# Kernel optimization log

Measured on AMD Instinct MI355X. Metric: run time of the kernel, lower is better.

Reference implementation:

```python
import jax, jax.numpy as jnp
import numpy as np

NEG_BIG = -9.0e15

def setup_inputs() -> dict:
    key = jax.random.key(0)
    k1, k2, k3, k4 = jax.random.split(key, 4)
    N, F_in, F_out = 2048, 512, 64
    x = jax.random.normal(k1, (N, F_in), dtype=jnp.float32)
    adj = jax.random.randint(k2, (N, N), 0, 2, dtype=jnp.int32)
    # xavier_uniform with gain=1.414
    def xavier(k, shape, gain=1.414):
        fan_in, fan_out = shape[0], shape[1]
        bound = gain * np.sqrt(6.0 / (fan_in + fan_out))
        return jax.random.uniform(k, shape, jnp.float32, -bound, bound)
    W = xavier(k3, (F_in, F_out))
    a = xavier(k4, (F_out, 1))
    return {"x": x, "adj": adj, "W": W, "a": a}

def reference(x, adj, W, a):
    h = x @ W                                  # [N, F_out]
    # pairwise |h_i - h_j| projected by a: e[i,j] = relu(sum_f |h_i,f - h_j,f| * a_f)
    diff = jnp.abs(h[:, None, :] - h[None, :, :])   # [N, N, F_out]
    e = jax.nn.relu(jnp.einsum('ijf,fo->ij', diff, a))  # [N, N]
    scores = jnp.where(adj > 0, e, NEG_BIG)
    attention = jax.nn.softmax(scores, axis=1)
    out = attention @ h                        # [N, F_out]
    return jax.nn.relu(out)                    # concat=True path
```

## Files before the change

kernel.cpp:

```cpp
#include <hip/hip_runtime.h>

#define Nn 2048
#define FIN 512
#define FO 64
#define SHIFT 20.0f
#define NJT 32
#define HS 68
#define PTS 68
#define ZTOT (Nn * FO + Nn)

#define HX(r, f) ((r) * HS + ((((f) >> 2) ^ (((r) >> 2) & 15)) << 2))

__global__ __launch_bounds__(256) void gat_xw(const float* __restrict__ x,
                                              const float* __restrict__ W,
                                              float* __restrict__ h,
                                              float* __restrict__ z) {
    const int gt = blockIdx.x * 256 + threadIdx.x;
    if (z != nullptr && gt < ZTOT) z[gt] = 0.f;

    __shared__ float part[2][2][FO];
    const int wave = threadIdx.x >> 6;
    const int lane = threadIdx.x & 63;
    const int rs = wave >> 1;
    const int kh = wave & 1;
    int row = blockIdx.x * 2 + rs;
    row = __builtin_amdgcn_readfirstlane(row);
    const float* xr = x + (size_t)row * FIN + kh * (FIN / 2);
    const float* Wp = W + (size_t)kh * (FIN / 2) * FO;
    float acc = 0.f;
#pragma unroll 2
    for (int k = 0; k < FIN / 2; k += 8) {
        float4 xa = *(const float4*)(xr + k);
        float4 xb = *(const float4*)(xr + k + 4);
        acc = fmaf(xa.x, Wp[(k + 0) * FO + lane], acc);
        acc = fmaf(xa.y, Wp[(k + 1) * FO + lane], acc);
        acc = fmaf(xa.z, Wp[(k + 2) * FO + lane], acc);
        acc = fmaf(xa.w, Wp[(k + 3) * FO + lane], acc);
        acc = fmaf(xb.x, Wp[(k + 4) * FO + lane], acc);
        acc = fmaf(xb.y, Wp[(k + 5) * FO + lane], acc);
        acc = fmaf(xb.z, Wp[(k + 6) * FO + lane], acc);
        acc = fmaf(xb.w, Wp[(k + 7) * FO + lane], acc);
    }
    part[rs][kh][lane] = acc;
    __syncthreads();
    if (threadIdx.x < 128) {
        const int r2 = threadIdx.x >> 6;
        const int l2 = threadIdx.x & 63;
        h[((size_t)blockIdx.x * 2 + r2) * FO + l2] = part[r2][0][l2] + part[r2][1][l2];
    }
}

template <bool ATOMIC>
__global__ __launch_bounds__(256, 4) void gat_attn6(const float* __restrict__ h,
                                                    const int* __restrict__ adj,
                                                    const float* __restrict__ a,
                                                    float* __restrict__ po,
                                                    float* __restrict__ pl) {
    __shared__ __align__(16) float hj_s[64 * HS];
    __shared__ __align__(16) float pT_s[64 * PTS];

    const int tid = threadIdx.x;
    const int w = tid >> 6;
    const int lane = tid & 63;
    const int li = lane & 3;
    const int lj = lane >> 2;
    const int it = blockIdx.x >> 5;
    const int jt = blockIdx.x & (NJT - 1);
    const int ib = it * 64;
    const int jb = jt * 64;
    const int iw = w * 16;

    for (int g4 = tid; g4 < 1024; g4 += 256) {
        const int row = g4 >> 4;
        const int f0 = (g4 & 15) * 4;
        float4 u = *(const float4*)(h + (size_t)jb * FO + (size_t)g4 * 4);
        *(float4*)&hj_s[HX(row, f0)] = u;
    }
    __syncthreads();

    float e[4][4];
#pragma unroll
    for (int di = 0; di < 4; di++)
#pragma unroll
        for (int dj = 0; dj < 4; dj++) e[di][dj] = 0.f;

    const float* hib = h + (size_t)(ib + iw + 4 * li) * FO;

#pragma unroll 4
    for (int f4 = 0; f4 < 16; f4++) {
        const float4 av = *(const float4*)(a + f4 * 4);
        float4 hi4[4], hj4[4];
#pragma unroll
        for (int d = 0; d < 4; d++) {
            hi4[d] = *(const float4*)(hib + (size_t)d * FO + f4 * 4);
            hj4[d] = *(const float4*)&hj_s[HX(4 * lj + d, f4 * 4)];
        }
#pragma unroll
        for (int di = 0; di < 4; di++)
#pragma unroll
            for (int dj = 0; dj < 4; dj++) {
                e[di][dj] = fmaf(fabsf(hi4[di].x - hj4[dj].x), av.x, e[di][dj]);
                e[di][dj] = fmaf(fabsf(hi4[di].y - hj4[dj].y), av.y, e[di][dj]);
                e[di][dj] = fmaf(fabsf(hi4[di].z - hj4[dj].z), av.z, e[di][dj]);
                e[di][dj] = fmaf(fabsf(hi4[di].w - hj4[dj].w), av.w, e[di][dj]);
            }
    }

    float ls[4];
#pragma unroll
    for (int di = 0; di < 4; di++) ls[di] = 0.f;
#pragma unroll
    for (int di = 0; di < 4; di++) {
        const int4 am = *(const int4*)(adj + (size_t)(ib + iw + 4 * li + di) * Nn + (jb + 4 * lj));
        const int* ap = (const int*)&am;
#pragma unroll
        for (int dj = 0; dj < 4; dj++) {
            const float p = (ap[dj] > 0) ? __expf(fmaxf(e[di][dj], 0.f) - SHIFT) : 0.f;
            e[di][dj] = p;
            ls[di] += p;
        }
    }

#pragma unroll
    for (int dj = 0; dj < 4; dj++) {
        *(float4*)&pT_s[(4 * lj + dj) * PTS + iw + 4 * li] =
            make_float4(e[0][dj], e[1][dj], e[2][dj], e[3][dj]);
    }

    float pv[4][4];
#pragma unroll
    for (int u = 0; u < 4; u++)
#pragma unroll
        for (int v2 = 0; v2 < 4; v2++) pv[u][v2] = 0.f;

#pragma unroll 4
    for (int j = 0; j < 64; j++) {
        const float4 pj = *(const float4*)&pT_s[j * PTS + iw + 4 * li];
        const float4 hv = *(const float4*)(h + (size_t)(jb + j) * FO + 4 * lj);
        pv[0][0] = fmaf(pj.x, hv.x, pv[0][0]);
        pv[0][1] = fmaf(pj.x, hv.y, pv[0][1]);
        pv[0][2] = fmaf(pj.x, hv.z, pv[0][2]);
        pv[0][3] = fmaf(pj.x, hv.w, pv[0][3]);
        pv[1][0] = fmaf(pj.y, hv.x, pv[1][0]);
        pv[1][1] = fmaf(pj.y, hv.y, pv[1][1]);
        pv[1][2] = fmaf(pj.y, hv.z, pv[1][2]);
        pv[1][3] = fmaf(pj.y, hv.w, pv[1][3]);
        pv[2][0] = fmaf(pj.z, hv.x, pv[2][0]);
        pv[2][1] = fmaf(pj.z, hv.y, pv[2][1]);
        pv[2][2] = fmaf(pj.z, hv.z, pv[2][2]);
        pv[2][3] = fmaf(pj.z, hv.w, pv[2][3]);
        pv[3][0] = fmaf(pj.w, hv.x, pv[3][0]);
        pv[3][1] = fmaf(pj.w, hv.y, pv[3][1]);
        pv[3][2] = fmaf(pj.w, hv.z, pv[3][2]);
        pv[3][3] = fmaf(pj.w, hv.w, pv[3][3]);
    }

#pragma unroll
    for (int di = 0; di < 4; di++) {
        float v = ls[di];
        v += __shfl_xor(v, 4, 64);
        v += __shfl_xor(v, 8, 64);
        v += __shfl_xor(v, 16, 64);
        v += __shfl_xor(v, 32, 64);
        ls[di] = v;
    }

    if constexpr (!ATOMIC) {
        if (lj == 0) {
#pragma unroll
            for (int di = 0; di < 4; di++)
                pl[(size_t)jt * Nn + (ib + iw + 4 * li + di)] = ls[di];
        }
#pragma unroll
        for (int di = 0; di < 4; di++)
            *(float4*)&po[((size_t)jt * Nn + (ib + iw + 4 * li + di)) * FO + 4 * lj] =
                make_float4(pv[di][0], pv[di][1], pv[di][2], pv[di][3]);
    } else {
        if (lj == 0) {
#pragma unroll
            for (int di = 0; di < 4; di++)
                atomicAdd(&pl[ib + iw + 4 * li + di], ls[di]);
        }
#pragma unroll
        for (int di = 0; di < 4; di++) {
#pragma unroll
            for (int v2 = 0; v2 < 4; v2++)
                atomicAdd(&po[(size_t)(ib + iw + 4 * li + di) * FO + 4 * lj + v2], pv[di][v2]);
        }
    }
}

__global__ __launch_bounds__(256) void gat_reduce(const float* __restrict__ po,
                                                  const float* __restrict__ pl,
                                                  float* __restrict__ out) {
    const int t = blockIdx.x * 256 + threadIdx.x;
    const int i = t >> 6;
    float s = 0.f;
#pragma unroll
    for (int p = 0; p < NJT; p++) s += po[(size_t)p * (Nn * FO) + t];
    float l = 0.f;
#pragma unroll
    for (int p = 0; p < NJT; p++) l += pl[p * Nn + i];
    out[t] = fmaxf(s / l, 0.f);
}

__global__ __launch_bounds__(256) void gat_fin(const float* __restrict__ osum,
                                               const float* __restrict__ lsum,
                                               float* __restrict__ out) {
    const int t = blockIdx.x * 256 + threadIdx.x;
    out[t] = fmaxf(osum[t] / lsum[t >> 6], 0.f);
}

extern "C" void kernel_launch(void* const* d_in, const int* in_sizes, int n_in,
                              void* d_out, int out_size, void* d_ws, size_t ws_size,
                              hipStream_t stream) {
    const float* x   = (const float*)d_in[0];
    const int*   adj = (const int*)d_in[1];
    const float* W   = (const float*)d_in[2];
    const float* a   = (const float*)d_in[3];
    float* out = (float*)d_out;

    float* h = (float*)d_ws;
    const size_t need = ((size_t)Nn * FO + (size_t)NJT * Nn * FO + (size_t)NJT * Nn) * 4;

    if (ws_size >= need) {
        float* po = h + (size_t)Nn * FO;
        float* pl = po + (size_t)NJT * Nn * FO;
        gat_xw<<<dim3(1024), dim3(256), 0, stream>>>(x, W, h, nullptr);
        gat_attn6<false><<<dim3(32 * NJT), dim3(256), 0, stream>>>(h, adj, a, po, pl);
        gat_reduce<<<dim3(512), dim3(256), 0, stream>>>(po, pl, out);
    } else {
        float* osum = h + (size_t)Nn * FO;
        float* lsum = osum + (size_t)Nn * FO;
        gat_xw<<<dim3(1024), dim3(256), 0, stream>>>(x, W, h, osum);
        gat_attn6<true><<<dim3(32 * NJT), dim3(256), 0, stream>>>(h, adj, a, osum, lsum);
        gat_fin<<<dim3(512), dim3(256), 0, stream>>>(osum, lsum, out);
    }
}
```

Measured before the change: 133.7 us.

## Enlarge attention i-tile to 128 rows and stage hi, a, and hj in LDS

The attention kernel now covers 128 query rows per block instead of 64, and each thread computes an 8x4 score tile instead of 4x4. The h_i rows, the vector a, and the h_j rows used in the P·V product are now staged in shared memory, so the per-thread global loads go away and each loaded h_j tile is reused across twice as many rows. The P^T buffer reuses the h_i region behind an extra barrier and gets a new XOR swizzle. In exchange the block count halves (512 blocks), register pressure roughly doubles under the launch bounds of 4 waves, and shared-memory use per block grows, which may cut occupancy.

```diff
diff --git a/kernel.cpp b/kernel.cpp
--- a/kernel.cpp
+++ b/kernel.cpp
@@ -6,10 +6,12 @@
 #define SHIFT 20.0f
 #define NJT 32
 #define HS 68
-#define PTS 68
+#define PTS2 132
 #define ZTOT (Nn * FO + Nn)
 
-#define HX(r, f) ((r) * HS + ((((f) >> 2) ^ (((r) >> 2) & 15)) << 2))
+#define HXI(r, f) ((r) * HS + ((((f) >> 2) ^ (((r) >> 3) & 15)) << 2))
+#define HXJ(r, f) ((r) * HS + ((((f) >> 2) ^ (((r) >> 2) & 15)) << 2))
+#define PX(j, i)  ((j) * PTS2 + ((((i) >> 2) ^ ((j) & 7)) << 2))
 
 __global__ __launch_bounds__(256) void gat_xw(const float* __restrict__ x,
                                               const float* __restrict__ W,
@@ -51,13 +53,16 @@
 }
 
 template <bool ATOMIC>
-__global__ __launch_bounds__(256, 4) void gat_attn6(const float* __restrict__ h,
+__global__ __launch_bounds__(256, 4) void gat_attn7(const float* __restrict__ h,
                                                     const int* __restrict__ adj,
                                                     const float* __restrict__ a,
                                                     float* __restrict__ po,
                                                     float* __restrict__ pl) {
+    __shared__ __align__(16) float up[128 * HS];
     __shared__ __align__(16) float hj_s[64 * HS];
-    __shared__ __align__(16) float pT_s[64 * PTS];
+    __shared__ float a_s[FO];
+    float* hi_s = up;
+    float* pT_s = up;
 
     const int tid = threadIdx.x;
     const int w = tid >> 6;
@@ -66,37 +71,39 @@
     const int lj = lane >> 2;
     const int it = blockIdx.x >> 5;
     const int jt = blockIdx.x & (NJT - 1);
-    const int ib = it * 64;
+    const int ib = it * 128;
     const int jb = jt * 64;
-    const int iw = w * 16;
-
+    const int i0 = 32 * w + 8 * li;
+
+    for (int g4 = tid; g4 < 2048; g4 += 256) {
+        const int row = g4 >> 4;
+        const int f0 = (g4 & 15) * 4;
+        *(float4*)&hi_s[HXI(row, f0)] = *(const float4*)(h + (size_t)ib * FO + (size_t)g4 * 4);
+    }
     for (int g4 = tid; g4 < 1024; g4 += 256) {
         const int row = g4 >> 4;
         const int f0 = (g4 & 15) * 4;
-        float4 u = *(const float4*)(h + (size_t)jb * FO + (size_t)g4 * 4);
-        *(float4*)&hj_s[HX(row, f0)] = u;
-    }
+        *(float4*)&hj_s[HXJ(row, f0)] = *(const float4*)(h + (size_t)jb * FO + (size_t)g4 * 4);
+    }
+    if (tid < FO) a_s[tid] = a[tid];
     __syncthreads();
 
-    float e[4][4];
-#pragma unroll
-    for (int di = 0; di < 4; di++)
+    float e[8][4];
+#pragma unroll
+    for (int di = 0; di < 8; di++)
 #pragma unroll
         for (int dj = 0; dj < 4; dj++) e[di][dj] = 0.f;
-
-    const float* hib = h + (size_t)(ib + iw + 4 * li) * FO;
 
 #pragma unroll 4
     for (int f4 = 0; f4 < 16; f4++) {
-        const float4 av = *(const float4*)(a + f4 * 4);
-        float4 hi4[4], hj4[4];
-#pragma unroll
-        for (int d = 0; d < 4; d++) {
-            hi4[d] = *(const float4*)(hib + (size_t)d * FO + f4 * 4);
-            hj4[d] = *(const float4*)&hj_s[HX(4 * lj + d, f4 * 4)];
-        }
-#pragma unroll
-        for (int di = 0; di < 4; di++)
+        const float4 av = *(const float4*)&a_s[f4 * 4];
+        float4 hi4[8], hj4[4];
+#pragma unroll
+        for (int d = 0; d < 8; d++) hi4[d] = *(const float4*)&hi_s[HXI(i0 + d, f4 * 4)];
+#pragma unroll
+        for (int d = 0; d < 4; d++) hj4[d] = *(const float4*)&hj_s[HXJ(4 * lj + d, f4 * 4)];
+#pragma unroll
+        for (int di = 0; di < 8; di++)
 #pragma unroll
             for (int dj = 0; dj < 4; dj++) {
                 e[di][dj] = fmaf(fabsf(hi4[di].x - hj4[dj].x), av.x, e[di][dj]);
@@ -106,12 +113,12 @@
             }
     }
 
-    float ls[4];
-#pragma unroll
-    for (int di = 0; di < 4; di++) ls[di] = 0.f;
-#pragma unroll
-    for (int di = 0; di < 4; di++) {
-        const int4 am = *(const int4*)(adj + (size_t)(ib + iw + 4 * li + di) * Nn + (jb + 4 * lj));
+    float ls[8];
+#pragma unroll
+    for (int di = 0; di < 8; di++) ls[di] = 0.f;
+#pragma unroll
+    for (int di = 0; di < 8; di++) {
+        const int4 am = *(const int4*)(adj + (size_t)(ib + i0 + di) * Nn + (jb + 4 * lj));
         const int* ap = (const int*)&am;
 #pragma unroll
         for (int dj = 0; dj < 4; dj++) {
@@ -121,42 +128,48 @@
         }
     }
 
+    __syncthreads();
+
 #pragma unroll
     for (int dj = 0; dj < 4; dj++) {
-        *(float4*)&pT_s[(4 * lj + dj) * PTS + iw + 4 * li] =
+        const int j = 4 * lj + dj;
+        *(float4*)&pT_s[PX(j, i0)] =
             make_float4(e[0][dj], e[1][dj], e[2][dj], e[3][dj]);
-    }
-
-    float pv[4][4];
-#pragma unroll
-    for (int u = 0; u < 4; u++)
-#pragma unroll
-        for (int v2 = 0; v2 < 4; v2++) pv[u][v2] = 0.f;
+        *(float4*)&pT_s[PX(j, i0 + 4)] =
+            make_float4(e[4][dj], e[5][dj], e[6][dj], e[7][dj]);
+    }
+
+    float pv[8][4];
+#pragma unroll
+    for (int di = 0; di < 8; di++)
+#pragma unroll
+        for (int c = 0; c < 4; c++) pv[di][c] = 0.f;
 
 #pragma unroll 4
     for (int j = 0; j < 64; j++) {
-        const float4 pj = *(const float4*)&pT_s[j * PTS + iw + 4 * li];
-        const float4 hv = *(const float4*)(h + (size_t)(jb + j) * FO + 4 * lj);
-        pv[0][0] = fmaf(pj.x, hv.x, pv[0][0]);
-        pv[0][1] = fmaf(pj.x, hv.y, pv[0][1]);
-        pv[0][2] = fmaf(pj.x, hv.z, pv[0][2]);
-        pv[0][3] = fmaf(pj.x, hv.w, pv[0][3]);
-        pv[1][0] = fmaf(pj.y, hv.x, pv[1][0]);
-        pv[1][1] = fmaf(pj.y, hv.y, pv[1][1]);
-        pv[1][2] = fmaf(pj.y, hv.z, pv[1][2]);
-        pv[1][3] = fmaf(pj.y, hv.w, pv[1][3]);
-        pv[2][0] = fmaf(pj.z, hv.x, pv[2][0]);
-        pv[2][1] = fmaf(pj.z, hv.y, pv[2][1]);
-        pv[2][2] = fmaf(pj.z, hv.z, pv[2][2]);
-        pv[2][3] = fmaf(pj.z, hv.w, pv[2][3]);
-        pv[3][0] = fmaf(pj.w, hv.x, pv[3][0]);
-        pv[3][1] = fmaf(pj.w, hv.y, pv[3][1]);
-        pv[3][2] = fmaf(pj.w, hv.z, pv[3][2]);
-        pv[3][3] = fmaf(pj.w, hv.w, pv[3][3]);
-    }
-
-#pragma unroll
-    for (int di = 0; di < 4; di++) {
+        const float4 pj0 = *(const float4*)&pT_s[PX(j, i0)];
+        const float4 pj1 = *(const float4*)&pT_s[PX(j, i0 + 4)];
+        const float4 hv = *(const float4*)&hj_s[HXJ(j, 4 * lj)];
+        pv[0][0] = fmaf(pj0.x, hv.x, pv[0][0]); pv[0][1] = fmaf(pj0.x, hv.y, pv[0][1]);
+        pv[0][2] = fmaf(pj0.x, hv.z, pv[0][2]); pv[0][3] = fmaf(pj0.x, hv.w, pv[0][3]);
+        pv[1][0] = fmaf(pj0.y, hv.x, pv[1][0]); pv[1][1] = fmaf(pj0.y, hv.y, pv[1][1]);
+        pv[1][2] = fmaf(pj0.y, hv.z, pv[1][2]); pv[1][3] = fmaf(pj0.y, hv.w, pv[1][3]);
+        pv[2][0] = fmaf(pj0.z, hv.x, pv[2][0]); pv[2][1] = fmaf(pj0.z, hv.y, pv[2][1]);
+        pv[2][2] = fmaf(pj0.z, hv.z, pv[2][2]); pv[2][3] = fmaf(pj0.z, hv.w, pv[2][3]);
+        pv[3][0] = fmaf(pj0.w, hv.x, pv[3][0]); pv[3][1] = fmaf(pj0.w, hv.y, pv[3][1]);
+        pv[3][2] = fmaf(pj0.w, hv.z, pv[3][2]); pv[3][3] = fmaf(pj0.w, hv.w, pv[3][3]);
+        pv[4][0] = fmaf(pj1.x, hv.x, pv[4][0]); pv[4][1] = fmaf(pj1.x, hv.y, pv[4][1]);
+        pv[4][2] = fmaf(pj1.x, hv.z, pv[4][2]); pv[4][3] = fmaf(pj1.x, hv.w, pv[4][3]);
+        pv[5][0] = fmaf(pj1.y, hv.x, pv[5][0]); pv[5][1] = fmaf(pj1.y, hv.y, pv[5][1]);
+        pv[5][2] = fmaf(pj1.y, hv.z, pv[5][2]); pv[5][3] = fmaf(pj1.y, hv.w, pv[5][3]);
+        pv[6][0] = fmaf(pj1.z, hv.x, pv[6][0]); pv[6][1] = fmaf(pj1.z, hv.y, pv[6][1]);
+        pv[6][2] = fmaf(pj1.z, hv.z, pv[6][2]); pv[6][3] = fmaf(pj1.z, hv.w, pv[6][3]);
+        pv[7][0] = fmaf(pj1.w, hv.x, pv[7][0]); pv[7][1] = fmaf(pj1.w, hv.y, pv[7][1]);
+        pv[7][2] = fmaf(pj1.w, hv.z, pv[7][2]); pv[7][3] = fmaf(pj1.w, hv.w, pv[7][3]);
+    }
+
+#pragma unroll
+    for (int di = 0; di < 8; di++) {
         float v = ls[di];
         v += __shfl_xor(v, 4, 64);
         v += __shfl_xor(v, 8, 64);
@@ -168,24 +181,24 @@
     if constexpr (!ATOMIC) {
         if (lj == 0) {
 #pragma unroll
-            for (int di = 0; di < 4; di++)
-                pl[(size_t)jt * Nn + (ib + iw + 4 * li + di)] = ls[di];
-        }
-#pragma unroll
-        for (int di = 0; di < 4; di++)
-            *(float4*)&po[((size_t)jt * Nn + (ib + iw + 4 * li + di)) * FO + 4 * lj] =
+            for (int di = 0; di < 8; di++)
+                pl[(size_t)jt * Nn + (ib + i0 + di)] = ls[di];
+        }
+#pragma unroll
+        for (int di = 0; di < 8; di++)
+            *(float4*)&po[((size_t)jt * Nn + (ib + i0 + di)) * FO + 4 * lj] =
                 make_float4(pv[di][0], pv[di][1], pv[di][2], pv[di][3]);
     } else {
         if (lj == 0) {
 #pragma unroll
-            for (int di = 0; di < 4; di++)
-                atomicAdd(&pl[ib + iw + 4 * li + di], ls[di]);
-        }
-#pragma unroll
-        for (int di = 0; di < 4; di++) {
-#pragma unroll
-            for (int v2 = 0; v2 < 4; v2++)
-                atomicAdd(&po[(size_t)(ib + iw + 4 * li + di) * FO + 4 * lj + v2], pv[di][v2]);
+            for (int di = 0; di < 8; di++)
+                atomicAdd(&pl[ib + i0 + di], ls[di]);
+        }
+#pragma unroll
+        for (int di = 0; di < 8; di++) {
+#pragma unroll
+            for (int c = 0; c < 4; c++)
+                atomicAdd(&po[(size_t)(ib + i0 + di) * FO + 4 * lj + c], pv[di][c]);
         }
     }
 }
@@ -227,13 +240,13 @@
         float* po = h + (size_t)Nn * FO;
         float* pl = po + (size_t)NJT * Nn * FO;
         gat_xw<<<dim3(1024), dim3(256), 0, stream>>>(x, W, h, nullptr);
-        gat_attn6<false><<<dim3(32 * NJT), dim3(256), 0, stream>>>(h, adj, a, po, pl);
+        gat_attn7<false><<<dim3(16 * NJT), dim3(256), 0, stream>>>(h, adj, a, po, pl);
         gat_reduce<<<dim3(512), dim3(256), 0, stream>>>(po, pl, out);
     } else {
         float* osum = h + (size_t)Nn * FO;
         float* lsum = osum + (size_t)Nn * FO;
         gat_xw<<<dim3(1024), dim3(256), 0, stream>>>(x, W, h, osum);
-        gat_attn6<true><<<dim3(32 * NJT), dim3(256), 0, stream>>>(h, adj, a, osum, lsum);
+        gat_attn7<true><<<dim3(16 * NJT), dim3(256), 0, stream>>>(h, adj, a, osum, lsum);
         gat_fin<<<dim3(512), dim3(256), 0, stream>>>(osum, lsum, out);
     }
 }
```

Measured after the change: 121.5 us. -9.1%, faster.

## Exploit symmetry of pairwise L1 scores to compute each tile pair once

Applied to the files above, without the earlier changes.

The score e[i,j] depends on |h_i - h_j|, so it is symmetric. The kernel now launches only upper-triangular tile pairs and reuses each computed e tile for both (i,j) and (j,i), masking with adj and adj-transposed. The block index is mapped to (it,jt) with a triangular-number inversion. Both h tiles are now staged in shared memory so the PV products read h from LDS, which raises LDS use per block to four 64x68 buffers and may reduce occupancy. Off-diagonal blocks now do twice the PV work and an extra adj transpose read, with a second pass after a barrier.

```diff
diff --git a/kernel.cpp b/kernel.cpp
--- a/kernel.cpp
+++ b/kernel.cpp
@@ -4,7 +4,8 @@
 #define FIN 512
 #define FO 64
 #define SHIFT 20.0f
-#define NJT 32
+#define NP 32
+#define NB ((NP * (NP + 1)) / 2)
 #define HS 68
 #define PTS 68
 #define ZTOT (Nn * FO + Nn)
@@ -51,21 +52,29 @@
 }
 
 template <bool ATOMIC>
-__global__ __launch_bounds__(256, 4) void gat_attn6(const float* __restrict__ h,
+__global__ __launch_bounds__(256, 4) void gat_attn9(const float* __restrict__ h,
                                                     const int* __restrict__ adj,
                                                     const float* __restrict__ a,
                                                     float* __restrict__ po,
                                                     float* __restrict__ pl) {
+    __shared__ __align__(16) float hi_s[64 * HS];
     __shared__ __align__(16) float hj_s[64 * HS];
-    __shared__ __align__(16) float pT_s[64 * PTS];
+    __shared__ __align__(16) float pTa[64 * PTS];
+    __shared__ __align__(16) float pTb[64 * PTS];
+    __shared__ float a_s[FO];
+
+    const int b = blockIdx.x;
+    int it = (int)((65.0f - sqrtf(4225.0f - 8.0f * (float)b)) * 0.5f);
+    while ((it + 1) * NP - (((it + 1) * it) >> 1) <= b) it++;
+    while (it * NP - ((it * (it - 1)) >> 1) > b) it--;
+    const int jt = it + (b - (it * NP - ((it * (it - 1)) >> 1)));
+    const bool diag = (it == jt);
 
     const int tid = threadIdx.x;
     const int w = tid >> 6;
     const int lane = tid & 63;
     const int li = lane & 3;
     const int lj = lane >> 2;
-    const int it = blockIdx.x >> 5;
-    const int jt = blockIdx.x & (NJT - 1);
     const int ib = it * 64;
     const int jb = jt * 64;
     const int iw = w * 16;
@@ -73,9 +82,10 @@
     for (int g4 = tid; g4 < 1024; g4 += 256) {
         const int row = g4 >> 4;
         const int f0 = (g4 & 15) * 4;
-        float4 u = *(const float4*)(h + (size_t)jb * FO + (size_t)g4 * 4);
-        *(float4*)&hj_s[HX(row, f0)] = u;
-    }
+        *(float4*)&hi_s[HX(row, f0)] = *(const float4*)(h + (size_t)ib * FO + (size_t)g4 * 4);
+        *(float4*)&hj_s[HX(row, f0)] = *(const float4*)(h + (size_t)jb * FO + (size_t)g4 * 4);
+    }
+    if (tid < FO) a_s[tid] = a[tid];
     __syncthreads();
 
     float e[4][4];
@@ -83,16 +93,14 @@
     for (int di = 0; di < 4; di++)
 #pragma unroll
         for (int dj = 0; dj < 4; dj++) e[di][dj] = 0.f;
-
-    const float* hib = h + (size_t)(ib + iw + 4 * li) * FO;
 
 #pragma unroll 4
     for (int f4 = 0; f4 < 16; f4++) {
-        const float4 av = *(const float4*)(a + f4 * 4);
+        const float4 av = *(const float4*)&a_s[f4 * 4];
         float4 hi4[4], hj4[4];
 #pragma unroll
         for (int d = 0; d < 4; d++) {
-            hi4[d] = *(const float4*)(hib + (size_t)d * FO + f4 * 4);
+            hi4[d] = *(const float4*)&hi_s[HX(iw + 4 * li + d, f4 * 4)];
             hj4[d] = *(const float4*)&hj_s[HX(4 * lj + d, f4 * 4)];
         }
 #pragma unroll
@@ -106,25 +114,42 @@
             }
     }
 
-    float ls[4];
-#pragma unroll
-    for (int di = 0; di < 4; di++) ls[di] = 0.f;
+#pragma unroll
+    for (int di = 0; di < 4; di++)
+#pragma unroll
+        for (int dj = 0; dj < 4; dj++)
+            e[di][dj] = __expf(fmaxf(e[di][dj], 0.f) - SHIFT);
+
+    int4 ama[4];
+#pragma unroll
+    for (int di = 0; di < 4; di++)
+        ama[di] = *(const int4*)(adj + (size_t)(ib + iw + 4 * li + di) * Nn + (jb + 4 * lj));
+#define PA(di, dj) ((((const int*)&ama[di])[dj] > 0) ? e[di][dj] : 0.f)
+
+    float lsa[4];
 #pragma unroll
     for (int di = 0; di < 4; di++) {
-        const int4 am = *(const int4*)(adj + (size_t)(ib + iw + 4 * li + di) * Nn + (jb + 4 * lj));
-        const int* ap = (const int*)&am;
-#pragma unroll
-        for (int dj = 0; dj < 4; dj++) {
-            const float p = (ap[dj] > 0) ? __expf(fmaxf(e[di][dj], 0.f) - SHIFT) : 0.f;
-            e[di][dj] = p;
-            ls[di] += p;
-        }
-    }
-
+        lsa[di] = 0.f;
+#pragma unroll
+        for (int dj = 0; dj < 4; dj++) lsa[di] += PA(di, dj);
+    }
 #pragma unroll
     for (int dj = 0; dj < 4; dj++) {
-        *(float4*)&pT_s[(4 * lj + dj) * PTS + iw + 4 * li] =
-            make_float4(e[0][dj], e[1][dj], e[2][dj], e[3][dj]);
+        *(float4*)&pTa[(4 * lj + dj) * PTS + iw + 4 * li] =
+            make_float4(PA(0, dj), PA(1, dj), PA(2, dj), PA(3, dj));
+    }
+
+    if (!diag) {
+        int4 amb[4];
+#pragma unroll
+        for (int dj = 0; dj < 4; dj++)
+            amb[dj] = *(const int4*)(adj + (size_t)(jb + 4 * lj + dj) * Nn + (ib + iw + 4 * li));
+#define PB(di, dj) ((((const int*)&amb[dj])[di] > 0) ? e[di][dj] : 0.f)
+#pragma unroll
+        for (int di = 0; di < 4; di++) {
+            *(float4*)&pTb[(iw + 4 * li + di) * PTS + 4 * lj] =
+                make_float4(PB(di, 0), PB(di, 1), PB(di, 2), PB(di, 3));
+        }
     }
 
     float pv[4][4];
@@ -135,41 +160,32 @@
 
 #pragma unroll 4
     for (int j = 0; j < 64; j++) {
-        const float4 pj = *(const float4*)&pT_s[j * PTS + iw + 4 * li];
-        const float4 hv = *(const float4*)(h + (size_t)(jb + j) * FO + 4 * lj);
-        pv[0][0] = fmaf(pj.x, hv.x, pv[0][0]);
-        pv[0][1] = fmaf(pj.x, hv.y, pv[0][1]);
-        pv[0][2] = fmaf(pj.x, hv.z, pv[0][2]);
-        pv[0][3] = fmaf(pj.x, hv.w, pv[0][3]);
-        pv[1][0] = fmaf(pj.y, hv.x, pv[1][0]);
-        pv[1][1] = fmaf(pj.y, hv.y, pv[1][1]);
-        pv[1][2] = fmaf(pj.y, hv.z, pv[1][2]);
-        pv[1][3] = fmaf(pj.y, hv.w, pv[1][3]);
-        pv[2][0] = fmaf(pj.z, hv.x, pv[2][0]);
-        pv[2][1] = fmaf(pj.z, hv.y, pv[2][1]);
-        pv[2][2] = fmaf(pj.z, hv.z, pv[2][2]);
-        pv[2][3] = fmaf(pj.z, hv.w, pv[2][3]);
-        pv[3][0] = fmaf(pj.w, hv.x, pv[3][0]);
-        pv[3][1] = fmaf(pj.w, hv.y, pv[3][1]);
-        pv[3][2] = fmaf(pj.w, hv.z, pv[3][2]);
-        pv[3][3] = fmaf(pj.w, hv.w, pv[3][3]);
+        const float4 pj = *(const float4*)&pTa[j * PTS + iw + 4 * li];
+        const float4 hv = *(const float4*)&hj_s[HX(j, 4 * lj)];
+        pv[0][0] = fmaf(pj.x, hv.x, pv[0][0]); pv[0][1] = fmaf(pj.x, hv.y, pv[0][1]);
+        pv[0][2] = fmaf(pj.x, hv.z, pv[0][2]); pv[0][3] = fmaf(pj.x, hv.w, pv[0][3]);
+        pv[1][0] = fmaf(pj.y, hv.x, pv[1][0]); pv[1][1] = fmaf(pj.y, hv.y, pv[1][1]);
+        pv[1][2] = fmaf(pj.y, hv.z, pv[1][2]); pv[1][3] = fmaf(pj.y, hv.w, pv[1][3]);
+        pv[2][0] = fmaf(pj.z, hv.x, pv[2][0]); pv[2][1] = fmaf(pj.z, hv.y, pv[2][1]);
+        pv[2][2] = fmaf(pj.z, hv.z, pv[2][2]); pv[2][3] = fmaf(pj.z, hv.w, pv[2][3]);
+        pv[3][0] = fmaf(pj.w, hv.x, pv[3][0]); pv[3][1] = fmaf(pj.w, hv.y, pv[3][1]);
+        pv[3][2] = fmaf(pj.w, hv.z, pv[3][2]); pv[3][3] = fmaf(pj.w, hv.w, pv[3][3]);
     }
 
 #pragma unroll
     for (int di = 0; di < 4; di++) {
-        float v = ls[di];
+        float v = lsa[di];
         v += __shfl_xor(v, 4, 64);
         v += __shfl_xor(v, 8, 64);
         v += __shfl_xor(v, 16, 64);
         v += __shfl_xor(v, 32, 64);
-        ls[di] = v;
-    }
-
+        lsa[di] = v;
+    }
     if constexpr (!ATOMIC) {
         if (lj == 0) {
 #pragma unroll
             for (int di = 0; di < 4; di++)
-                pl[(size_t)jt * Nn + (ib + iw + 4 * li + di)] = ls[di];
+                pl[(size_t)jt * Nn + (ib + iw + 4 * li + di)] = lsa[di];
         }
 #pragma unroll
         for (int di = 0; di < 4; di++)
@@ -179,7 +195,7 @@
         if (lj == 0) {
 #pragma unroll
             for (int di = 0; di < 4; di++)
-                atomicAdd(&pl[ib + iw + 4 * li + di], ls[di]);
+                atomicAdd(&pl[ib + iw + 4 * li + di], lsa[di]);
         }
 #pragma unroll
         for (int di = 0; di < 4; di++) {
@@ -188,6 +204,60 @@
                 atomicAdd(&po[(size_t)(ib + iw + 4 * li + di) * FO + 4 * lj + v2], pv[di][v2]);
         }
     }
+
+    if (!diag) {
+        __syncthreads();
+
+        float pvb[4][4];
+        float lsb[4];
+#pragma unroll
+        for (int u = 0; u < 4; u++) {
+            lsb[u] = 0.f;
+#pragma unroll
+            for (int v2 = 0; v2 < 4; v2++) pvb[u][v2] = 0.f;
+        }
+
+#pragma unroll 4
+        for (int i = 0; i < 64; i++) {
+            const float4 pj = *(const float4*)&pTb[i * PTS + iw + 4 * li];
+            const float4 hv = *(const float4*)&hi_s[HX(i, 4 * lj)];
+            lsb[0] += pj.x; lsb[1] += pj.y; lsb[2] += pj.z; lsb[3] += pj.w;
+            pvb[0][0] = fmaf(pj.x, hv.x, pvb[0][0]); pvb[0][1] = fmaf(pj.x, hv.y, pvb[0][1]);
+            pvb[0][2] = fmaf(pj.x, hv.z, pvb[0][2]); pvb[0][3] = fmaf(pj.x, hv.w, pvb[0][3]);
+            pvb[1][0] = fmaf(pj.y, hv.x, pvb[1][0]); pvb[1][1] = fmaf(pj.y, hv.y, pvb[1][1]);
+            pvb[1][2] = fmaf(pj.y, hv.z, pvb[1][2]); pvb[1][3] = fmaf(pj.y, hv.w, pvb[1][3]);
+            pvb[2][0] = fmaf(pj.z, hv.x, pvb[2][0]); pvb[2][1] = fmaf(pj.z, hv.y, pvb[2][1]);
+            pvb[2][2] = fmaf(pj.z, hv.z, pvb[2][2]); pvb[2][3] = fmaf(pj.z, hv.w, pvb[2][3]);
+            pvb[3][0] = fmaf(pj.w, hv.x, pvb[3][0]); pvb[3][1] = fmaf(pj.w, hv.y, pvb[3][1]);
+            pvb[3][2] = fmaf(pj.w, hv.z, pvb[3][2]); pvb[3][3] = fmaf(pj.w, hv.w, pvb[3][3]);
+        }
+
+        if constexpr (!ATOMIC) {
+            if (lj == 0) {
+#pragma unroll
+                for (int d = 0; d < 4; d++)
+                    pl[(size_t)it * Nn + (jb + iw + 4 * li + d)] = lsb[d];
+            }
+#pragma unroll
+            for (int d = 0; d < 4; d++)
+                *(float4*)&po[((size_t)it * Nn + (jb + iw + 4 * li + d)) * FO + 4 * lj] =
+                    make_float4(pvb[d][0], pvb[d][1], pvb[d][2], pvb[d][3]);
+        } else {
+            if (lj == 0) {
+#pragma unroll
+                for (int d = 0; d < 4; d++)
+                    atomicAdd(&pl[jb + iw + 4 * li + d], lsb[d]);
+            }
+#pragma unroll
+            for (int d = 0; d < 4; d++) {
+#pragma unroll
+                for (int v2 = 0; v2 < 4; v2++)
+                    atomicAdd(&po[(size_t)(jb + iw + 4 * li + d) * FO + 4 * lj + v2], pvb[d][v2]);
+            }
+        }
+    }
+#undef PA
+#undef PB
 }
 
 __global__ __launch_bounds__(256) void gat_reduce(const float* __restrict__ po,
@@ -197,10 +267,10 @@
     const int i = t >> 6;
     float s = 0.f;
 #pragma unroll
-    for (int p = 0; p < NJT; p++) s += po[(size_t)p * (Nn * FO) + t];
+    for (int p = 0; p < NP; p++) s += po[(size_t)p * (Nn * FO) + t];
     float l = 0.f;
 #pragma unroll
-    for (int p = 0; p < NJT; p++) l += pl[p * Nn + i];
+    for (int p = 0; p < NP; p++) l += pl[p * Nn + i];
     out[t] = fmaxf(s / l, 0.f);
 }
 
@@ -221,19 +291,19 @@
     float* out = (float*)d_out;
 
     float* h = (float*)d_ws;
-    const size_t need = ((size_t)Nn * FO + (size_t)NJT * Nn * FO + (size_t)NJT * Nn) * 4;
+    const size_t need = ((size_t)Nn * FO + (size_t)NP * Nn * FO + (size_t)NP * Nn) * 4;
 
     if (ws_size >= need) {
         float* po = h + (size_t)Nn * FO;
-        float* pl = po + (size_t)NJT * Nn * FO;
+        float* pl = po + (size_t)NP * Nn * FO;
         gat_xw<<<dim3(1024), dim3(256), 0, stream>>>(x, W, h, nullptr);
-        gat_attn6<false><<<dim3(32 * NJT), dim3(256), 0, stream>>>(h, adj, a, po, pl);
+        gat_attn9<false><<<dim3(NB), dim3(256), 0, stream>>>(h, adj, a, po, pl);
         gat_reduce<<<dim3(512), dim3(256), 0, stream>>>(po, pl, out);
     } else {
         float* osum = h + (size_t)Nn * FO;
         float* lsum = osum + (size_t)Nn * FO;
         gat_xw<<<dim3(1024), dim3(256), 0, stream>>>(x, W, h, osum);
-        gat_attn6<true><<<dim3(32 * NJT), dim3(256), 0, stream>>>(h, adj, a, osum, lsum);
+        gat_attn9<true><<<dim3(NB), dim3(256), 0, stream>>>(h, adj, a, osum, lsum);
         gat_fin<<<dim3(512), dim3(256), 0, stream>>>(osum, lsum, out);
     }
 }
```

Result: faster. 118.7 us (-11.2%).

## Store hj and attention tiles as bf16 in LDS, raise occupancy

Applied to the files above, without the earlier changes.

The j-tile of h and the transposed probability tile now live in shared memory as packed bf16 with a new XOR swizzle, halving LDS footprint. The PV loop reads h_j from LDS instead of global memory, and `a` is staged in LDS. Launch bounds go from 4 to 6 blocks per CU to use the freed LDS. This trades precision (bf16 rounding of h_j in both the score and PV stages, and of the probabilities) and extra unpack ALU work for less LDS traffic and higher occupancy.

```diff
diff --git a/kernel.cpp b/kernel.cpp
--- a/kernel.cpp
+++ b/kernel.cpp
@@ -5,11 +5,19 @@
 #define FO 64
 #define SHIFT 20.0f
 #define NJT 32
-#define HS 68
-#define PTS 68
+#define PBS2 72
 #define ZTOT (Nn * FO + Nn)
 
-#define HX(r, f) ((r) * HS + ((((f) >> 2) ^ (((r) >> 2) & 15)) << 2))
+#define HJX(r, f) ((r) * PBS2 + ((((f) >> 3) ^ (((r) >> 2) & 7)) << 3) + ((f) & 7))
+#define PX16(j, i) ((j) * PBS2 + ((((i) >> 3) ^ ((j) & 7)) << 3) + ((i) & 7))
+
+__device__ __forceinline__ unsigned pk2(float x, float y) {
+    unsigned r;
+    asm("v_cvt_pk_bf16_f32 %0, %1, %2" : "=v"(r) : "v"(x), "v"(y));
+    return r;
+}
+__device__ __forceinline__ float bflo(unsigned u) { return __uint_as_float(u << 16); }
+__device__ __forceinline__ float bfhi(unsigned u) { return __uint_as_float(u & 0xffff0000u); }
 
 __global__ __launch_bounds__(256) void gat_xw(const float* __restrict__ x,
                                               const float* __restrict__ W,
@@ -51,13 +59,14 @@
 }
 
 template <bool ATOMIC>
-__global__ __launch_bounds__(256, 4) void gat_attn6(const float* __restrict__ h,
-                                                    const int* __restrict__ adj,
-                                                    const float* __restrict__ a,
-                                                    float* __restrict__ po,
-                                                    float* __restrict__ pl) {
-    __shared__ __align__(16) float hj_s[64 * HS];
-    __shared__ __align__(16) float pT_s[64 * PTS];
+__global__ __launch_bounds__(256, 6) void gat_attn10(const float* __restrict__ h,
+                                                     const int* __restrict__ adj,
+                                                     const float* __restrict__ a,
+                                                     float* __restrict__ po,
+                                                     float* __restrict__ pl) {
+    __shared__ __align__(16) short hj16[64 * PBS2];
+    __shared__ __align__(16) short pT16[64 * PBS2];
+    __shared__ float a_s[FO];
 
     const int tid = threadIdx.x;
     const int w = tid >> 6;
@@ -73,9 +82,13 @@
     for (int g4 = tid; g4 < 1024; g4 += 256) {
         const int row = g4 >> 4;
         const int f0 = (g4 & 15) * 4;
-        float4 u = *(const float4*)(h + (size_t)jb * FO + (size_t)g4 * 4);
-        *(float4*)&hj_s[HX(row, f0)] = u;
-    }
+        const float4 u = *(const float4*)(h + (size_t)jb * FO + (size_t)g4 * 4);
+        uint2 pk;
+        pk.x = pk2(u.x, u.y);
+        pk.y = pk2(u.z, u.w);
+        *(uint2*)&hj16[HJX(row, f0)] = pk;
+    }
+    if (tid < FO) a_s[tid] = a[tid];
     __syncthreads();
 
     float e[4][4];
@@ -88,12 +101,14 @@
 
 #pragma unroll 4
     for (int f4 = 0; f4 < 16; f4++) {
-        const float4 av = *(const float4*)(a + f4 * 4);
+        const float4 av = *(const float4*)&a_s[f4 * 4];
         float4 hi4[4], hj4[4];
 #pragma unroll
         for (int d = 0; d < 4; d++) {
             hi4[d] = *(const float4*)(hib + (size_t)d * FO + f4 * 4);
-            hj4[d] = *(const float4*)&hj_s[HX(4 * lj + d, f4 * 4)];
+            const uint2 hw = *(const uint2*)&hj16[HJX(4 * lj + d, f4 * 4)];
+            hj4[d].x = bflo(hw.x); hj4[d].y = bfhi(hw.x);
+            hj4[d].z = bflo(hw.y); hj4[d].w = bfhi(hw.y);
         }
 #pragma unroll
         for (int di = 0; di < 4; di++)
@@ -120,11 +135,12 @@
             ls[di] += p;
         }
     }
-
 #pragma unroll
     for (int dj = 0; dj < 4; dj++) {
-        *(float4*)&pT_s[(4 * lj + dj) * PTS + iw + 4 * li] =
-            make_float4(e[0][dj], e[1][dj], e[2][dj], e[3][dj]);
+        uint2 pk;
+        pk.x = pk2(e[0][dj], e[1][dj]);
+        pk.y = pk2(e[2][dj], e[3][dj]);
+        *(uint2*)&pT16[PX16(4 * lj + dj, iw + 4 * li)] = pk;
     }
 
     float pv[4][4];
@@ -135,24 +151,18 @@
 
 #pragma unroll 4
     for (int j = 0; j < 64; j++) {
-        const float4 pj = *(const float4*)&pT_s[j * PTS + iw + 4 * li];
-        const float4 hv = *(const float4*)(h + (size_t)(jb + j) * FO + 4 * lj);
-        pv[0][0] = fmaf(pj.x, hv.x, pv[0][0]);
-        pv[0][1] = fmaf(pj.x, hv.y, pv[0][1]);
-        pv[0][2] = fmaf(pj.x, hv.z, pv[0][2]);
-        pv[0][3] = fmaf(pj.x, hv.w, pv[0][3]);
-        pv[1][0] = fmaf(pj.y, hv.x, pv[1][0]);
-        pv[1][1] = fmaf(pj.y, hv.y, pv[1][1]);
-        pv[1][2] = fmaf(pj.y, hv.z, pv[1][2]);
-        pv[1][3] = fmaf(pj.y, hv.w, pv[1][3]);
-        pv[2][0] = fmaf(pj.z, hv.x, pv[2][0]);
-        pv[2][1] = fmaf(pj.z, hv.y, pv[2][1]);
-        pv[2][2] = fmaf(pj.z, hv.z, pv[2][2]);
-        pv[2][3] = fmaf(pj.z, hv.w, pv[2][3]);
-        pv[3][0] = fmaf(pj.w, hv.x, pv[3][0]);
-        pv[3][1] = fmaf(pj.w, hv.y, pv[3][1]);
-        pv[3][2] = fmaf(pj.w, hv.z, pv[3][2]);
-        pv[3][3] = fmaf(pj.w, hv.w, pv[3][3]);
+        const uint2 pw = *(const uint2*)&pT16[PX16(j, iw + 4 * li)];
+        const uint2 hw = *(const uint2*)&hj16[HJX(j, 4 * lj)];
+        const float p0 = bflo(pw.x), p1 = bfhi(pw.x), p2 = bflo(pw.y), p3 = bfhi(pw.y);
+        const float h0 = bflo(hw.x), h1 = bfhi(hw.x), h2 = bflo(hw.y), h3 = bfhi(hw.y);
+        pv[0][0] = fmaf(p0, h0, pv[0][0]); pv[0][1] = fmaf(p0, h1, pv[0][1]);
+        pv[0][2] = fmaf(p0, h2, pv[0][2]); pv[0][3] = fmaf(p0, h3, pv[0][3]);
+        pv[1][0] = fmaf(p1, h0, pv[1][0]); pv[1][1] = fmaf(p1, h1, pv[1][1]);
+        pv[1][2] = fmaf(p1, h2, pv[1][2]); pv[1][3] = fmaf(p1, h3, pv[1][3]);
+        pv[2][0] = fmaf(p2, h0, pv[2][0]); pv[2][1] = fmaf(p2, h1, pv[2][1]);
+        pv[2][2] = fmaf(p2, h2, pv[2][2]); pv[2][3] = fmaf(p2, h3, pv[2][3]);
+        pv[3][0] = fmaf(p3, h0, pv[3][0]); pv[3][1] = fmaf(p3, h1, pv[3][1]);
+        pv[3][2] = fmaf(p3, h2, pv[3][2]); pv[3][3] = fmaf(p3, h3, pv[3][3]);
     }
 
 #pragma unroll
@@ -227,13 +237,13 @@
         float* po = h + (size_t)Nn * FO;
         float* pl = po + (size_t)NJT * Nn * FO;
         gat_xw<<<dim3(1024), dim3(256), 0, stream>>>(x, W, h, nullptr);
-        gat_attn6<false><<<dim3(32 * NJT), dim3(256), 0, stream>>>(h, adj, a, po, pl);
+        gat_attn10<false><<<dim3(32 * NJT), dim3(256), 0, stream>>>(h, adj, a, po, pl);
         gat_reduce<<<dim3(512), dim3(256), 0, stream>>>(po, pl, out);
     } else {
         float* osum = h + (size_t)Nn * FO;
         float* lsum = osum + (size_t)Nn * FO;
         gat_xw<<<dim3(1024), dim3(256), 0, stream>>>(x, W, h, osum);
-        gat_attn6<true><<<dim3(32 * NJT), dim3(256), 0, stream>>>(h, adj, a, osum, lsum);
+        gat_attn10<true><<<dim3(32 * NJT), dim3(256), 0, stream>>>(h, adj, a, osum, lsum);
         gat_fin<<<dim3(512), dim3(256), 0, stream>>>(osum, lsum, out);
     }
 }
```

Measured after the change: 197.1 us. +47.5%, slower.
